# Optimization experiments

Hardware: AMD Instinct MI355X
Metric: run time of the kernel (lower is better)

The kernel has to match this reference:

```python
import jax, jax.numpy as jnp
import numpy as np

B, N0, D, H = 64, 512, 512, 2048  # graphs, nodes/graph, d_hidden, mlp hidden


def _mlp(x, W1, b1, W2, b2, W3, b3):
    h = jax.nn.relu(x @ W1 + b1)
    h = jax.nn.relu(h @ W2 + b2)
    return h @ W3 + b3


def setup_inputs() -> dict:
    key = jax.random.key(0)
    ks = jax.random.split(key, 16)
    total = B * N0
    x = jax.random.normal(ks[0], (total, D), jnp.float32)
    node_type = jax.random.randint(ks[1], (total,), 0, 4, jnp.int32)
    action_mask = jax.random.bernoulli(ks[2], 0.5, (total,))
    node_indices = jnp.tile(jnp.arange(N0, dtype=jnp.int32), B)
    batch = jnp.repeat(jnp.arange(B, dtype=jnp.int32), N0)
    N = jnp.full((B,), N0, dtype=jnp.int32)

    def lin(k, fan_in, fan_out):
        kw, kb = jax.random.split(k)
        bound = 1.0 / np.sqrt(fan_in)
        W = jax.random.uniform(kw, (fan_in, fan_out), jnp.float32, -bound, bound)
        b = jax.random.uniform(kb, (fan_out,), jnp.float32, -bound, bound)
        return W, b

    mlp_W1, mlp_b1 = lin(ks[3], D, H)
    mlp_W2, mlp_b2 = lin(ks[4], H, H)
    mlp_W3, mlp_b3 = lin(ks[5], H, 1)
    vf_W1, vf_b1 = lin(ks[6], D, H)
    vf_W2, vf_b2 = lin(ks[7], H, H)
    vf_W3, vf_b3 = lin(ks[8], H, 1)
    return dict(x=x, node_type=node_type, action_mask=action_mask,
                node_indices=node_indices, batch=batch, N=N,
                mlp_W1=mlp_W1, mlp_b1=mlp_b1, mlp_W2=mlp_W2, mlp_b2=mlp_b2,
                mlp_W3=mlp_W3, mlp_b3=mlp_b3,
                vf_W1=vf_W1, vf_b1=vf_b1, vf_W2=vf_W2, vf_b2=vf_b2,
                vf_W3=vf_W3, vf_b3=vf_b3)


def reference(x, node_type, action_mask, node_indices, batch, N,
              mlp_W1, mlp_b1, mlp_W2, mlp_b2, mlp_W3, mlp_b3,
              vf_W1, vf_b1, vf_W2, vf_b2, vf_W3, vf_b3):
    nb = N.shape[0]
    # global mean pool over graphs
    counts = jax.ops.segment_sum(jnp.ones((x.shape[0],), x.dtype), batch, num_segments=nb)
    h_mean = jax.ops.segment_sum(x, batch, num_segments=nb) / counts[:, None]
    # masked gather -> MLP -> scatter with -inf fill, expressed as masked select
    z_node = _mlp(x, mlp_W1, mlp_b1, mlp_W2, mlp_b2, mlp_W3, mlp_b3)[:, 0]
    z_all = jnp.where(action_mask, z_node, -jnp.inf)
    z = z_all.reshape(nb, -1)  # multi_length=False: all graphs have N[0] nodes
    v = _mlp(h_mean, vf_W1, vf_b1, vf_W2, vf_b2, vf_W3, vf_b3)
    return z, v
```

## Files before the change

kernel.cpp:

```cpp
#include <hip/hip_runtime.h>
#include <cstdint>
#include <cmath>


typedef __bf16 bf16_t;
typedef float  f32x4  __attribute__((ext_vector_type(4)));
typedef int    i32x4  __attribute__((ext_vector_type(4)));
typedef int    i32x8  __attribute__((ext_vector_type(8)));

#define NB      64
#define N0      512
#define DIM     512
#define HID     2048
#define TOTAL   32768
#define ZNEG    -3.0e38f

__device__ __forceinline__ void gload16(const void* g, void* l) {
  __builtin_amdgcn_global_load_lds(
      (const uint32_t __attribute__((address_space(1)))*)g,
      (uint32_t __attribute__((address_space(3)))*)l, 16, 0, 0);
}

__device__ __forceinline__ unsigned char to_fp8(float f) {
  return (unsigned char)(__builtin_amdgcn_cvt_pk_fp8_f32(f, f, 0, false) & 0xff);
}

__global__ void mask_scan_kernel(const unsigned char* __restrict__ mask,
                                 int* __restrict__ perm,
                                 int* __restrict__ pos,
                                 int* __restrict__ mcount) {
  __shared__ int ts[1024];
  const int t = threadIdx.x;
  const uint32_t* m32 = (const uint32_t*)mask;
  uint32_t w[8];
  int s = 0;
#pragma unroll
  for (int k = 0; k < 8; ++k) {
    w[k] = m32[t * 8 + k];
    s += __popc(w[k] & 0x01010101u);
  }
  ts[t] = s;
  __syncthreads();
  for (int off = 1; off < 1024; off <<= 1) {
    int v = (t >= off) ? ts[t - off] : 0;
    __syncthreads();
    ts[t] += v;
    __syncthreads();
  }
  int run = ts[t] - s;
  const int base = t * 32;
#pragma unroll
  for (int k = 0; k < 32; ++k) {
    int bit = (w[k >> 2] >> ((k & 3) * 8)) & 1;
    if (bit) {
      perm[run] = base + k;
      pos[base + k] = run;
      run++;
    }
  }
  if (t == 1023) {
    mcount[0] = ts[1023];
    mcount[1] = (ts[1023] + 127) & ~127;
  }
}

__global__ void gather_fp8_kernel(const float* __restrict__ x,
                                  const int* __restrict__ perm,
                                  const int* __restrict__ mcount,
                                  uint32_t* __restrict__ xc) {
  const int idx = blockIdx.x * 256 + threadIdx.x;
  const int r = idx >> 7;
  const int c = idx & 127;
  if (r >= mcount[1]) return;
  uint32_t v = 0;
  if (r < mcount[0]) {
    const float4 f = ((const float4*)(x + (size_t)perm[r] * DIM))[c];
    int p = __builtin_amdgcn_cvt_pk_fp8_f32(f.x, f.y, 0, false);
    p = __builtin_amdgcn_cvt_pk_fp8_f32(f.z, f.w, p, true);
    v = (uint32_t)p;
  }
  xc[idx] = v;
}


__global__ void transpose_to_fp8_kernel(const float* __restrict__ W,
                                        uint8_t* __restrict__ Wt,
                                        int K, int N, float scale) {
  __shared__ float tile[32][33];
  const int bx = blockIdx.x;
  const int by = blockIdx.y;
  const int tx = threadIdx.x & 31;
  const int ty = threadIdx.x >> 5;
#pragma unroll
  for (int r = 0; r < 4; ++r)
    tile[ty + r * 8][tx] = W[(size_t)(by * 32 + ty + r * 8) * N + bx * 32 + tx];
  __syncthreads();
#pragma unroll
  for (int r = 0; r < 4; ++r)
    Wt[(size_t)(bx * 32 + ty + r * 8) * K + by * 32 + tx] =
        to_fp8(tile[tx][ty + r * 8] * scale);
}

__global__ void zero_kernel(float* __restrict__ p, int n) {
  int i = blockIdx.x * 256 + threadIdx.x;
  if (i < n) p[i] = 0.f;
}

__global__ void hmean_accum_kernel(const float* __restrict__ x,
                                   float* __restrict__ hsumT) {
  const int g = blockIdx.x >> 3;
  const int slab = blockIdx.x & 7;
  const int c = threadIdx.x;
  const float* xp = x + ((size_t)g * N0 + slab * 64) * DIM + c;
  float s = 0.f;
#pragma unroll 8
  for (int r = 0; r < 64; ++r) s += xp[(size_t)r * DIM];
  atomicAdd(&hsumT[(size_t)c * NB + g], s);
}

__global__ void vf_partial_kernel(const float* __restrict__ h,
                                  const float* __restrict__ W,
                                  float* __restrict__ pacc,
                                  int kspan) {
  __shared__ float hs[64 * 64];
  const int tx = threadIdx.x & 31;
  const int ty = threadIdx.x >> 5;
  const int n0 = blockIdx.x * 128 + tx * 4;
  const int g0 = ty * 8;
  const int k0 = blockIdx.y * kspan;

  const float4* hsrc = (const float4*)(h + (size_t)k0 * NB);
  for (int i = threadIdx.x; i < (kspan << 4); i += 256)
    ((float4*)hs)[i] = hsrc[i];
  __syncthreads();

  float acc[8][4] = {};
  const float* wp = W + (size_t)k0 * HID + n0;
#pragma unroll 4
  for (int kk = 0; kk < kspan; ++kk) {
    const float4 w = *(const float4*)(wp + (size_t)kk * HID);
    const float* hr = hs + (kk << 6) + g0;
    const float4 ha = *(const float4*)hr;
    const float4 hb = *(const float4*)(hr + 4);
    const float hv[8] = {ha.x, ha.y, ha.z, ha.w, hb.x, hb.y, hb.z, hb.w};
#pragma unroll
    for (int r = 0; r < 8; ++r) {
      acc[r][0] += hv[r] * w.x;
      acc[r][1] += hv[r] * w.y;
      acc[r][2] += hv[r] * w.z;
      acc[r][3] += hv[r] * w.w;
    }
  }
#pragma unroll
  for (int r = 0; r < 8; ++r) {
    float4 o = {acc[r][0], acc[r][1], acc[r][2], acc[r][3]};
    *(float4*)(pacc + ((size_t)blockIdx.y * NB + g0 + r) * HID + n0) = o;
  }
}

__global__ void vf_l1_fin_kernel(const float* __restrict__ pacc1,
                                 const float* __restrict__ vb1,
                                 float* __restrict__ vh1t) {
  const int idx = blockIdx.x * 256 + threadIdx.x;
  const int g = idx >> 11;
  const int n = idx & 2047;
  float s = 0.f;
#pragma unroll
  for (int kg = 0; kg < 16; ++kg)
    s += pacc1[((size_t)kg * NB + g) * HID + n];
  vh1t[(size_t)n * NB + g] = fmaxf(s * (1.f / 512.f) + vb1[n], 0.f);
}

__global__ void vf_l23_fin_kernel(const float* __restrict__ pacc2,
                                  const float* __restrict__ vb2,
                                  const float* __restrict__ vW3,
                                  float* __restrict__ vfzp) {
  __shared__ float rs[4];
  const int g = blockIdx.x >> 3;
  const int n = (blockIdx.x & 7) * 256 + threadIdx.x;
  float s = 0.f;
#pragma unroll
  for (int kg = 0; kg < 32; ++kg)
    s += pacc2[((size_t)kg * NB + g) * HID + n];
  float t = fmaxf(s + vb2[n], 0.f) * vW3[n];
#pragma unroll
  for (int off = 32; off; off >>= 1) t += __shfl_down(t, off, 64);
  if ((threadIdx.x & 63) == 0) rs[threadIdx.x >> 6] = t;
  __syncthreads();
  if (threadIdx.x == 0)
    vfzp[g * 8 + (blockIdx.x & 7)] = rs[0] + rs[1] + rs[2] + rs[3];
}

template <int FUSE>
__global__ __launch_bounds__(256) void gemm_f8(
    const uint8_t* __restrict__ A, const uint8_t* __restrict__ Bt,
    const float* __restrict__ bias, const float* __restrict__ w3,
    uint8_t* __restrict__ C, float* __restrict__ zout,
    const int* __restrict__ mlim, int M, int N, int K, int sb) {
  const int bm = blockIdx.y;
  const int bn = blockIdx.x;
  if (bm * 128 >= *mlim) return;

  __shared__ __align__(16) char Asb[128 * 128];
  __shared__ __align__(16) char Bsb[128 * 128];

  const int tid = threadIdx.x;
  const int wave = tid >> 6;
  const int lane = tid & 63;
  const int lr = lane & 15;
  const int lq = lane >> 4;
  const int swz = lr & 7;
  const int wm = (wave >> 1) << 6;
  const int wn = (wave & 1) << 6;

  const int srow0 = (wave << 3) + (lane >> 3);
  const int gchunk = (lane & 7) ^ (lane >> 3);

  const uint8_t* ag = A + (size_t)(bm * 128 + srow0) * K + (gchunk << 4);
  const uint8_t* bg = Bt + (size_t)(bn * 128 + srow0) * K + (gchunk << 4);
  char* asw = Asb + (wave << 10);
  char* bsw = Bsb + (wave << 10);

  f32x4 acc[4][4] = {};

  for (int k0 = 0; k0 < K; k0 += 128) {
#pragma unroll
    for (int j = 0; j < 4; ++j) {
      gload16(ag + (size_t)(j * 32) * K, asw + j * 4096);
      gload16(bg + (size_t)(j * 32) * K, bsw + j * 4096);
    }
    ag += 128;
    bg += 128;
    __syncthreads();

    i32x8 a8[4], b8[4];
#pragma unroll
    for (int i = 0; i < 4; ++i) {
      const char* base = Asb + ((wm + i * 16 + lr) << 7);
      i32x4 lo = *(const i32x4*)(base + ((((lq << 1) | 0) ^ swz) << 4));
      i32x4 hi = *(const i32x4*)(base + ((((lq << 1) | 1) ^ swz) << 4));
      a8[i] = __builtin_shufflevector(lo, hi, 0, 1, 2, 3, 4, 5, 6, 7);
    }
#pragma unroll
    for (int j = 0; j < 4; ++j) {
      const char* base = Bsb + ((wn + j * 16 + lr) << 7);
      i32x4 lo = *(const i32x4*)(base + ((((lq << 1) | 0) ^ swz) << 4));
      i32x4 hi = *(const i32x4*)(base + ((((lq << 1) | 1) ^ swz) << 4));
      b8[j] = __builtin_shufflevector(lo, hi, 0, 1, 2, 3, 4, 5, 6, 7);
    }
#pragma unroll
    for (int i = 0; i < 4; ++i)
#pragma unroll
      for (int j = 0; j < 4; ++j)
        acc[i][j] = __builtin_amdgcn_mfma_scale_f32_16x16x128_f8f6f4(
            a8[i], b8[j], acc[i][j], 0 , 0 ,
            0, 127 , 0, sb);
    __syncthreads();
  }

  if (FUSE == 0) {
#pragma unroll
    for (int j = 0; j < 4; ++j) {
      const int gc = bn * 128 + wn + j * 16 + lr;
      const float bj = bias[gc];
#pragma unroll
      for (int i = 0; i < 4; ++i) {
        const int gr0 = bm * 128 + wm + i * 16 + lq * 4;
#pragma unroll
        for (int r = 0; r < 4; ++r) {
          float v = fmaxf(acc[i][j][r] + bj, 0.f);
          C[(size_t)(gr0 + r) * N + gc] = to_fp8(v);
        }
      }
    }
  } else {
    float rs[4][4] = {};
#pragma unroll
    for (int j = 0; j < 4; ++j) {
      const int gc = bn * 128 + wn + j * 16 + lr;
      const float bj = bias[gc];
      const float wj = w3[gc];
#pragma unroll
      for (int i = 0; i < 4; ++i)
#pragma unroll
        for (int r = 0; r < 4; ++r)
          rs[i][r] += fmaxf(acc[i][j][r] + bj, 0.f) * wj;
    }
#pragma unroll
    for (int off = 1; off < 16; off <<= 1) {
#pragma unroll
      for (int i = 0; i < 4; ++i)
#pragma unroll
        for (int r = 0; r < 4; ++r)
          rs[i][r] += __shfl_xor(rs[i][r], off, 64);
    }
    if (lr == 0) {
#pragma unroll
      for (int i = 0; i < 4; ++i)
#pragma unroll
        for (int r = 0; r < 4; ++r)
          atomicAdd(&zout[bm * 128 + wm + i * 16 + lq * 4 + r], rs[i][r]);
    }
  }
}

__global__ void finalize_kernel(const float* __restrict__ zp,
                                const float* __restrict__ vfzp,
                                const unsigned char* __restrict__ mask,
                                const int* __restrict__ pos,
                                const float* __restrict__ b3,
                                const float* __restrict__ vb3,
                                float* __restrict__ out) {
  int i = blockIdx.x * 256 + threadIdx.x;
  if (i < TOTAL) {
    out[i] = mask[i] ? (zp[pos[i]] + b3[0]) : ZNEG;
  } else if (i < TOTAL + NB) {
    int g = i - TOTAL;
    float v = 0.f;
#pragma unroll
    for (int b = 0; b < 8; ++b) v += vfzp[g * 8 + b];
    out[i] = v + vb3[0];
  }
}

extern "C" void kernel_launch(void* const* d_in, const int* in_sizes, int n_in,
                              void* d_out, int out_size, void* d_ws,
                              size_t ws_size, hipStream_t stream) {
  (void)in_sizes; (void)n_in; (void)out_size; (void)ws_size;
  const float* x    = (const float*)d_in[0];
  const unsigned char* mask = (const unsigned char*)d_in[2];
  const float* W1   = (const float*)d_in[6];
  const float* b1   = (const float*)d_in[7];
  const float* W2   = (const float*)d_in[8];
  const float* b2   = (const float*)d_in[9];
  const float* W3   = (const float*)d_in[10];
  const float* b3   = (const float*)d_in[11];
  const float* vW1  = (const float*)d_in[12];
  const float* vb1  = (const float*)d_in[13];
  const float* vW2  = (const float*)d_in[14];
  const float* vb2  = (const float*)d_in[15];
  const float* vW3  = (const float*)d_in[16];
  const float* vb3  = (const float*)d_in[17];
  float* out = (float*)d_out;

  char* p = (char*)d_ws;
  size_t off = 0;
  auto alloc = [&](size_t bytes) {
    void* r = p + off;
    off = (off + bytes + 255) & ~(size_t)255;
    return r;
  };
  uint8_t* x_f8  = (uint8_t*)alloc((size_t)TOTAL * DIM);
  uint8_t* W1t   = (uint8_t*)alloc((size_t)HID * DIM);
  uint8_t* W2t   = (uint8_t*)alloc((size_t)HID * HID);
  uint8_t* H1    = (uint8_t*)alloc((size_t)TOTAL * HID);
  float*   vh1t  = (float*)alloc((size_t)HID * NB * 4);
  float*   pacc1 = (float*)alloc((size_t)16 * NB * HID * 4);
  float*   pacc2 = (float*)alloc((size_t)32 * NB * HID * 4);
  float*   vfzp  = (float*)alloc((size_t)NB * 8 * 4);
  int*     perm  = (int*)alloc((size_t)TOTAL * 4);
  int*     pos   = (int*)alloc((size_t)TOTAL * 4);
  int*     mcount= (int*)alloc(256);
  float*   zreg  = (float*)alloc((size_t)(DIM * NB + TOTAL) * 4);
  float*   hsumT = zreg;
  float*   zpart = zreg + DIM * NB;

  mask_scan_kernel<<<1, 1024, 0, stream>>>(mask, perm, pos, mcount);
  gather_fp8_kernel<<<TOTAL * 128 / 256, 256, 0, stream>>>(
      x, perm, mcount, (uint32_t*)x_f8);

  transpose_to_fp8_kernel<<<dim3(HID / 32, DIM / 32), 256, 0, stream>>>(
      W1, W1t, DIM, HID, 16.f);
  transpose_to_fp8_kernel<<<dim3(HID / 32, HID / 32), 256, 0, stream>>>(
      W2, W2t, HID, HID, 32.f);
  const int nzero = DIM * NB + TOTAL;
  zero_kernel<<<(nzero + 255) / 256, 256, 0, stream>>>(zreg, nzero);

  hmean_accum_kernel<<<NB * 8, 512, 0, stream>>>(x, hsumT);

  vf_partial_kernel<<<dim3(16, 16), 256, 0, stream>>>(
      hsumT, vW1, pacc1, 32);
  vf_l1_fin_kernel<<<512, 256, 0, stream>>>(pacc1, vb1, vh1t);
  vf_partial_kernel<<<dim3(16, 32), 256, 0, stream>>>(
      vh1t, vW2, pacc2, 64);
  vf_l23_fin_kernel<<<512, 256, 0, stream>>>(pacc2, vb2, vW3, vfzp);

  gemm_f8<0><<<dim3(HID / 128, TOTAL / 128), 256, 0, stream>>>(
      x_f8, W1t, b1, nullptr, H1, nullptr, mcount + 1, TOTAL, HID, DIM, 123);
  gemm_f8<1><<<dim3(HID / 128, TOTAL / 128), 256, 0, stream>>>(
      H1, W2t, b2, W3, nullptr, zpart, mcount + 1, TOTAL, HID, HID, 122);

  finalize_kernel<<<(TOTAL + NB + 255) / 256, 256, 0, stream>>>(
      zpart, vfzp, mask, pos, b3, vb3, out);
}
```

Measured before the change: 273.7 us.

## Fuse pooling with fp8 gather, merge weight transposes, drop atomics in z output

```diff
diff --git a/kernel.cpp b/kernel.cpp
--- a/kernel.cpp
+++ b/kernel.cpp
@@ -28,9 +28,12 @@
 __global__ void mask_scan_kernel(const unsigned char* __restrict__ mask,
                                  int* __restrict__ perm,
                                  int* __restrict__ pos,
-                                 int* __restrict__ mcount) {
+                                 int* __restrict__ mcount,
+                                 float* __restrict__ hsumT,
+                                 uint32_t* __restrict__ xc) {
   __shared__ int ts[1024];
   const int t = threadIdx.x;
+  for (int i = t; i < DIM * NB; i += 1024) hsumT[i] = 0.f;
   const uint32_t* m32 = (const uint32_t*)mask;
   uint32_t w[8];
   int s = 0;
@@ -58,64 +61,63 @@
       run++;
     }
   }
+  const int cnt = ts[1023];
+  const int mpad = (cnt + 127) & ~127;
+  for (int i = cnt * 128 + t; i < mpad * 128; i += 1024) xc[i] = 0;
   if (t == 1023) {
-    mcount[0] = ts[1023];
-    mcount[1] = (ts[1023] + 127) & ~127;
-  }
-}
-
-__global__ void gather_fp8_kernel(const float* __restrict__ x,
-                                  const int* __restrict__ perm,
-                                  const int* __restrict__ mcount,
-                                  uint32_t* __restrict__ xc) {
-  const int idx = blockIdx.x * 256 + threadIdx.x;
-  const int r = idx >> 7;
-  const int c = idx & 127;
-  if (r >= mcount[1]) return;
-  uint32_t v = 0;
-  if (r < mcount[0]) {
-    const float4 f = ((const float4*)(x + (size_t)perm[r] * DIM))[c];
-    int p = __builtin_amdgcn_cvt_pk_fp8_f32(f.x, f.y, 0, false);
-    p = __builtin_amdgcn_cvt_pk_fp8_f32(f.z, f.w, p, true);
-    v = (uint32_t)p;
-  }
-  xc[idx] = v;
-}
-
-
-__global__ void transpose_to_fp8_kernel(const float* __restrict__ W,
-                                        uint8_t* __restrict__ Wt,
-                                        int K, int N, float scale) {
+    mcount[0] = cnt;
+    mcount[1] = mpad;
+  }
+}
+
+__global__ void pool_convert_kernel(const float* __restrict__ x,
+                                    const unsigned char* __restrict__ mask,
+                                    const int* __restrict__ pos,
+                                    float* __restrict__ hsumT,
+                                    uint32_t* __restrict__ xc) {
+  const int g = blockIdx.x >> 3;
+  const int slab = blockIdx.x & 7;
+  const int c4 = threadIdx.x;
+  const int row0 = g * N0 + slab * 64;
+  const float4* xp = (const float4*)x + (size_t)row0 * 128 + c4;
+  float4 s = {0.f, 0.f, 0.f, 0.f};
+#pragma unroll 8
+  for (int r = 0; r < 64; ++r) {
+    float4 v = xp[(size_t)r * 128];
+    s.x += v.x; s.y += v.y; s.z += v.z; s.w += v.w;
+    if (mask[row0 + r]) {
+      int p = __builtin_amdgcn_cvt_pk_fp8_f32(v.x, v.y, 0, false);
+      p = __builtin_amdgcn_cvt_pk_fp8_f32(v.z, v.w, p, true);
+      xc[(size_t)pos[row0 + r] * 128 + c4] = (uint32_t)p;
+    }
+  }
+  atomicAdd(&hsumT[(size_t)(c4 * 4 + 0) * NB + g], s.x);
+  atomicAdd(&hsumT[(size_t)(c4 * 4 + 1) * NB + g], s.y);
+  atomicAdd(&hsumT[(size_t)(c4 * 4 + 2) * NB + g], s.z);
+  atomicAdd(&hsumT[(size_t)(c4 * 4 + 3) * NB + g], s.w);
+}
+
+__global__ void transpose_both_kernel(const float* __restrict__ W1,
+                                      const float* __restrict__ W2,
+                                      uint8_t* __restrict__ W1t,
+                                      uint8_t* __restrict__ W2t) {
   __shared__ float tile[32][33];
+  int by = blockIdx.y;
+  const float* W; uint8_t* Wt; int K; float scale;
+  if (by < 16) { W = W1; Wt = W1t; K = DIM; scale = 16.f; }
+  else         { W = W2; Wt = W2t; K = HID; scale = 32.f; by -= 16; }
   const int bx = blockIdx.x;
-  const int by = blockIdx.y;
   const int tx = threadIdx.x & 31;
   const int ty = threadIdx.x >> 5;
 #pragma unroll
   for (int r = 0; r < 4; ++r)
-    tile[ty + r * 8][tx] = W[(size_t)(by * 32 + ty + r * 8) * N + bx * 32 + tx];
+    tile[ty + r * 8][tx] =
+        W[(size_t)(by * 32 + ty + r * 8) * HID + bx * 32 + tx];
   __syncthreads();
 #pragma unroll
   for (int r = 0; r < 4; ++r)
     Wt[(size_t)(bx * 32 + ty + r * 8) * K + by * 32 + tx] =
         to_fp8(tile[tx][ty + r * 8] * scale);
-}
-
-__global__ void zero_kernel(float* __restrict__ p, int n) {
-  int i = blockIdx.x * 256 + threadIdx.x;
-  if (i < n) p[i] = 0.f;
-}
-
-__global__ void hmean_accum_kernel(const float* __restrict__ x,
-                                   float* __restrict__ hsumT) {
-  const int g = blockIdx.x >> 3;
-  const int slab = blockIdx.x & 7;
-  const int c = threadIdx.x;
-  const float* xp = x + ((size_t)g * N0 + slab * 64) * DIM + c;
-  float s = 0.f;
-#pragma unroll 8
-  for (int r = 0; r < 64; ++r) s += xp[(size_t)r * DIM];
-  atomicAdd(&hsumT[(size_t)c * NB + g], s);
 }
 
 __global__ void vf_partial_kernel(const float* __restrict__ h,
@@ -299,12 +301,13 @@
       for (int i = 0; i < 4; ++i)
 #pragma unroll
         for (int r = 0; r < 4; ++r)
-          atomicAdd(&zout[bm * 128 + wm + i * 16 + lq * 4 + r], rs[i][r]);
-    }
-  }
-}
-
-__global__ void finalize_kernel(const float* __restrict__ zp,
+          zout[(size_t)(bm * 128 + wm + i * 16 + lq * 4 + r) * 16 + bn] =
+              rs[i][r];
+    }
+  }
+}
+
+__global__ void finalize_kernel(const float* __restrict__ zp16,
                                 const float* __restrict__ vfzp,
                                 const unsigned char* __restrict__ mask,
                                 const int* __restrict__ pos,
@@ -313,7 +316,18 @@
                                 float* __restrict__ out) {
   int i = blockIdx.x * 256 + threadIdx.x;
   if (i < TOTAL) {
-    out[i] = mask[i] ? (zp[pos[i]] + b3[0]) : ZNEG;
+    if (mask[i]) {
+      const float4* zp = (const float4*)(zp16 + (size_t)pos[i] * 16);
+      float s = 0.f;
+#pragma unroll
+      for (int q = 0; q < 4; ++q) {
+        float4 v = zp[q];
+        s += (v.x + v.y) + (v.z + v.w);
+      }
+      out[i] = s + b3[0];
+    } else {
+      out[i] = ZNEG;
+    }
   } else if (i < TOTAL + NB) {
     int g = i - TOTAL;
     float v = 0.f;
@@ -358,25 +372,17 @@
   float*   pacc1 = (float*)alloc((size_t)16 * NB * HID * 4);
   float*   pacc2 = (float*)alloc((size_t)32 * NB * HID * 4);
   float*   vfzp  = (float*)alloc((size_t)NB * 8 * 4);
+  float*   zp16  = (float*)alloc((size_t)TOTAL * 16 * 4);
   int*     perm  = (int*)alloc((size_t)TOTAL * 4);
   int*     pos   = (int*)alloc((size_t)TOTAL * 4);
   int*     mcount= (int*)alloc(256);
-  float*   zreg  = (float*)alloc((size_t)(DIM * NB + TOTAL) * 4);
-  float*   hsumT = zreg;
-  float*   zpart = zreg + DIM * NB;
-
-  mask_scan_kernel<<<1, 1024, 0, stream>>>(mask, perm, pos, mcount);
-  gather_fp8_kernel<<<TOTAL * 128 / 256, 256, 0, stream>>>(
-      x, perm, mcount, (uint32_t*)x_f8);
-
-  transpose_to_fp8_kernel<<<dim3(HID / 32, DIM / 32), 256, 0, stream>>>(
-      W1, W1t, DIM, HID, 16.f);
-  transpose_to_fp8_kernel<<<dim3(HID / 32, HID / 32), 256, 0, stream>>>(
-      W2, W2t, HID, HID, 32.f);
-  const int nzero = DIM * NB + TOTAL;
-  zero_kernel<<<(nzero + 255) / 256, 256, 0, stream>>>(zreg, nzero);
-
-  hmean_accum_kernel<<<NB * 8, 512, 0, stream>>>(x, hsumT);
+  float*   hsumT = (float*)alloc((size_t)DIM * NB * 4);
+
+  mask_scan_kernel<<<1, 1024, 0, stream>>>(mask, perm, pos, mcount, hsumT,
+                                           (uint32_t*)x_f8);
+  pool_convert_kernel<<<NB * 8, 128, 0, stream>>>(x, mask, pos, hsumT,
+                                                  (uint32_t*)x_f8);
+  transpose_both_kernel<<<dim3(64, 80), 256, 0, stream>>>(W1, W2, W1t, W2t);
 
   vf_partial_kernel<<<dim3(16, 16), 256, 0, stream>>>(
       hsumT, vW1, pacc1, 32);
@@ -388,8 +394,8 @@
   gemm_f8<0><<<dim3(HID / 128, TOTAL / 128), 256, 0, stream>>>(
       x_f8, W1t, b1, nullptr, H1, nullptr, mcount + 1, TOTAL, HID, DIM, 123);
   gemm_f8<1><<<dim3(HID / 128, TOTAL / 128), 256, 0, stream>>>(
-      H1, W2t, b2, W3, nullptr, zpart, mcount + 1, TOTAL, HID, HID, 122);
+      H1, W2t, b2, W3, nullptr, zp16, mcount + 1, TOTAL, HID, HID, 122);
 
   finalize_kernel<<<(TOTAL + NB + 255) / 256, 256, 0, stream>>>(
-      zpart, vfzp, mask, pos, b3, vb3, out);
-}
+      zp16, vfzp, mask, pos, b3, vb3, out);
+}
```

New measurement: 280.1 us. +2.4%, slower.
